# Optimization experiments

Measured on AMD Instinct MI355X. Metric: run time of the kernel, lower is better.

## Reference

```python
import jax, jax.numpy as jnp
import numpy as np
import math

H_HEADS = 4
SQRT_2_PI = math.sqrt(2.0 / math.pi)


def _gelu_tanh(x):
    return 0.5 * x * (1.0 + jnp.tanh(SQRT_2_PI * (x + 0.044715 * x ** 3)))


def _ln(x, g, b, eps=1e-5):
    mu = jnp.mean(x, axis=-1, keepdims=True)
    var = jnp.var(x, axis=-1, keepdims=True)
    return g * (x - mu) * jax.lax.rsqrt(var + eps) + b


def _forward(support_emb_mat, query_t, support_t, cls_embed, t_freq, t_phase,
             Wq, bq, Wk, bk, Wv, bv, Wo, bo, ln1_g, ln1_b, time_w,
             W1, b1, W2, b2, ln2_g, ln2_b, Wc, bc, bn_g, bn_b):
    B, F, MD = support_emb_mat.shape
    Q = query_t.shape[1]
    S = F + 1
    H = H_HEADS
    D = MD * H
    dph = D // H
    L = Wq.shape[0]
    BQ = B * Q

    # [CLS] + support sequence, feature-tiled to model_dim*num_heads
    cls = jnp.broadcast_to(cls_embed, (B, 1, MD))
    seq = jnp.concatenate([cls, support_emb_mat], axis=1)          # [B,S,MD]
    x = jnp.tile(seq, (1, 1, H))                                    # [B,S,D]
    x = jnp.broadcast_to(x[:, None], (B, Q, S, D)).reshape(BQ, S, D)

    # time sequence: [query_t_q, support_t...] per (b,q)
    sup = jnp.broadcast_to(support_t[:, None, :], (B, Q, F))
    t_seq = jnp.concatenate([query_t[..., None], sup], axis=-1).reshape(BQ, S)
    t_diff = t_seq[:, :, None] - t_seq[:, None, :]                  # [BQ,S,S]
    # time encoder: cos(t*freq + phase) -> [BQ,S,S,TD]
    t_emb = jnp.cos(t_diff[..., None] * t_freq + t_phase)

    # scale as in source: (dim_per_head // num_heads) ** -0.5
    scale = (dph // H) ** (-0.5)

    for l in range(L):
        bias = t_emb @ time_w[l]                                    # [BQ,S,S]
        add = jnp.tile(bias, (H, 1, 1))                             # [BQ*H,S,S]
        res = x
        # raw row-major reshape to (BQ*H, S, dph) exactly as torch .view
        q = (x @ Wq[l] + bq[l]).reshape(BQ * H, S, dph)
        k = (x @ Wk[l] + bk[l]).reshape(BQ * H, S, dph)
        v = (x @ Wv[l] + bv[l]).reshape(BQ * H, S, dph)
        attn = jax.nn.softmax(jnp.einsum('bsd,btd->bst', q, k) * scale + add, axis=-1)
        ctx = jnp.einsum('bst,btd->bsd', attn, v).reshape(BQ, S, D)
        out = _ln(res + ctx @ Wo[l] + bo[l], ln1_g[l], ln1_b[l])
        ffn = _gelu_tanh(out @ W1[l] + b1[l]) @ W2[l] + b2[l]
        x = _ln(out + ffn, ln2_g[l], ln2_b[l])

    # compress: Linear -> BatchNorm1d over seq channels (train mode) -> LeakyReLU
    h = x @ Wc + bc                                                 # [BQ,S,MD]
    mu = jnp.mean(h, axis=(0, 2), keepdims=True)
    var = jnp.var(h, axis=(0, 2), keepdims=True)
    h = bn_g[None, :, None] * (h - mu) * jax.lax.rsqrt(var + 1e-5) + bn_b[None, :, None]
    h = jnp.where(h >= 0, h, 0.01 * h)                              # LeakyReLU
    return h[:, 0, :].reshape(B, Q, MD)


def setup_inputs() -> dict:
    key = jax.random.key(0)
    ks = jax.random.split(key, 24)
    B, Q, F, MD = 128, 32, 7, 128
    H, L, FFN, TD = 4, 6, 2048, 32
    S = F + 1
    D = MD * H

    def nrm(k, shape, s=0.02):
        return jax.random.normal(k, shape, jnp.float32) * s

    inp = {
        'support_emb_mat': jax.random.normal(ks[0], (B, F, MD), jnp.float32),
        'query_t': jax.random.uniform(ks[1], (B, Q), jnp.float32) * 100.0,
        'support_t': jax.random.uniform(ks[2], (B, F), jnp.float32) * 100.0,
        'cls_embed': jax.random.uniform(ks[3], (1, MD), jnp.float32),
        't_freq': nrm(ks[4], (TD,), 1.0),
        't_phase': nrm(ks[5], (TD,), 1.0),
        'Wq': nrm(ks[6], (L, D, D)), 'bq': jnp.zeros((L, D)),
        'Wk': nrm(ks[7], (L, D, D)), 'bk': jnp.zeros((L, D)),
        'Wv': nrm(ks[8], (L, D, D)), 'bv': jnp.zeros((L, D)),
        'Wo': nrm(ks[9], (L, D, D)), 'bo': jnp.zeros((L, D)),
        'ln1_g': jnp.ones((L, D)), 'ln1_b': jnp.zeros((L, D)),
        'time_w': jnp.ones((L, TD)) * 0.001,
        'W1': nrm(ks[10], (L, D, FFN)), 'b1': jnp.zeros((L, FFN)),
        'W2': nrm(ks[11], (L, FFN, D)), 'b2': jnp.zeros((L, D)),
        'ln2_g': jnp.ones((L, D)), 'ln2_b': jnp.zeros((L, D)),
        'Wc': nrm(ks[12], (D, MD)), 'bc': jnp.zeros((MD,)),
        'bn_g': jnp.ones((S,)), 'bn_b': jnp.zeros((S,)),
    }
    return inp


def reference(support_emb_mat, query_t, support_t, cls_embed, t_freq, t_phase,
              Wq, bq, Wk, bk, Wv, bv, Wo, bo, ln1_g, ln1_b, time_w,
              W1, b1, W2, b2, ln2_g, ln2_b, Wc, bc, bn_g, bn_b):
    return _forward(support_emb_mat, query_t, support_t, cls_embed, t_freq, t_phase,
                    Wq, bq, Wk, bk, Wv, bv, Wo, bo, ln1_g, ln1_b, time_w,
                    W1, b1, W2, b2, ln2_g, ln2_b, Wc, bc, bn_g, bn_b)
```

## Files before the change

kernel.cpp:

```cpp
#include <hip/hip_runtime.h>
#include <hip/hip_bf16.h>

typedef _Float16 f16;
typedef __attribute__((ext_vector_type(8))) _Float16 f16x8;
typedef __attribute__((ext_vector_type(4))) _Float16 f16x4;
typedef __attribute__((ext_vector_type(4))) float f32x4;

#define DEVI __device__ __forceinline__

DEVI float ldf(const void* p, size_t i, int isf32) {
    if (isf32) return ((const float*)p)[i];
    unsigned int u = ((const unsigned short*)p)[i];
    union { unsigned int b; float f; } c; c.b = u << 16;
    return c.f;
}

DEVI void gld_lds16(const f16* g, f16* l) {
    __builtin_amdgcn_global_load_lds(
        (__attribute__((address_space(1))) void*)(g),
        (__attribute__((address_space(3))) void*)(l), 16, 0, 0);
}

__global__ void detect_dtype(const void* qt, int* flag) {
    if (threadIdx.x == 0 && blockIdx.x == 0) {
        const unsigned int* w = (const unsigned int*)qt;
        int cnt = 0;
        for (int i = 0; i < 64; ++i) {
            unsigned int lo = w[i] & 0xFFFFu;
            union { unsigned int b; float f; } c; c.b = lo << 16;
            if (c.f >= 1e-4f && c.f <= 100.5f) ++cnt;
        }
        *flag = (cnt >= 32) ? 0 : 1;
    }
}

__global__ __launch_bounds__(256)
void cvt_in(const void* __restrict__ src, float* __restrict__ dst, int n,
            const int* __restrict__ flag) {
    const int f32 = *flag;
    int i = blockIdx.x * 256 + threadIdx.x;
    if (i < n) dst[i] = ldf(src, i, f32);
}

__global__ __launch_bounds__(256)
void fill_out(float* out, float v) {
    out[blockIdx.x * 256 + threadIdx.x] = v;
}

template<int EPI>
__global__ __launch_bounds__(512, 2)
void gemm256(const f16* __restrict__ Ag, const f16* __restrict__ BTg,
             const float* __restrict__ biasg, void* __restrict__ outg,
             int NZ, int gridN, int N, int K, int lda,
             long zsB, long zsBias, long zsC)
{
    const int tid = threadIdx.x;
    const int w = tid >> 6, lane = tid & 63;
    const int wm = w >> 2, wn = w & 3;
    const int r16 = lane & 15, q4 = lane >> 4;

    const int cpx = gridDim.x >> 3;
    const int id  = (blockIdx.x & 7) * cpx + (blockIdx.x >> 3);

    const int nz   = id % NZ;
    const int mloc = id / NZ;
    const int z    = nz / gridN;
    const int nt   = nz - z * gridN;
    const int tm = mloc * 256, tn = nt * 256;

    const f16*   BT   = BTg + (size_t)z * zsB;
    const float* bias = biasg + (size_t)z * zsBias;
    const size_t zoffC = (size_t)z * zsC;

    __shared__ __align__(16) f16 smA[2][2][16][64][8];
    __shared__ __align__(16) f16 smB[2][2][16][64][8];

    const f16* gA[4]; const f16* gB[4];
#pragma unroll
    for (int t = 0; t < 4; ++t) {
        const int c = 4 * w + t, kk = c >> 4, rc = c & 15;
        gA[t] = Ag + (size_t)(tm + rc * 16 + r16) * lda + kk * 32 + q4 * 8;
        gB[t] = BT + (size_t)(tn + rc * 16 + r16) * K  + kk * 32 + q4 * 8;
    }
    f16* const smAbase = &smA[0][0][0][0][0];
    f16* const smBbase = &smB[0][0][0][0][0];
    const int coff = (4 * w) * 512;

    auto issue = [&](int kt, int buf) {
        const size_t o = (size_t)kt * 64;
        const int bo = buf * 16384 + coff;
#pragma unroll
        for (int t = 0; t < 4; ++t) {
            gld_lds16(gA[t] + o, smAbase + bo + t * 512);
            gld_lds16(gB[t] + o, smBbase + bo + t * 512);
        }
    };

    f32x4 acc[8][4];
#pragma unroll
    for (int i = 0; i < 8; ++i)
#pragma unroll
        for (int j = 0; j < 4; ++j) acc[i][j] = (f32x4)0.0f;

    const int iters = K >> 6;
    issue(0, 0);
    __builtin_amdgcn_s_waitcnt(0x0F70);
    __builtin_amdgcn_s_barrier();
    __asm__ __volatile__("" ::: "memory");

    for (int kt = 0; kt < iters; ++kt) {
        const int cur = kt & 1;
        const bool more = (kt + 1 < iters);
        if (more) issue(kt + 1, cur ^ 1);
#pragma unroll
        for (int kk = 0; kk < 2; ++kk) {
            f16x8 af[8], bf[4];
#pragma unroll
            for (int i = 0; i < 8; ++i)
                af[i] = *(const f16x8*)&smA[cur][kk][wm * 8 + i][lane][0];
#pragma unroll
            for (int j = 0; j < 4; ++j)
                bf[j] = *(const f16x8*)&smB[cur][kk][wn * 4 + j][lane][0];
#pragma unroll
            for (int i = 0; i < 8; ++i)
#pragma unroll
                for (int j = 0; j < 4; ++j)
                    acc[i][j] = __builtin_amdgcn_mfma_f32_16x16x32_f16(
                        bf[j], af[i], acc[i][j], 0, 0, 0);
        }
        if (more) {
            __builtin_amdgcn_s_waitcnt(0x0F70);
            __builtin_amdgcn_s_barrier();
            __asm__ __volatile__("" ::: "memory");
        }
    }

    const int rowBase = tm + wm * 128;
    const int colBase = tn + wn * 64;
#pragma unroll
    for (int i = 0; i < 8; ++i) {
        const int row = rowBase + i * 16 + r16;
        const size_t rowoff = (size_t)row * N;
#pragma unroll
        for (int j = 0; j < 4; ++j) {
            const int n0 = colBase + j * 16 + q4 * 4;
            const f32x4 bv4 = *(const f32x4*)&bias[n0];
            f16x4 o;
#pragma unroll
            for (int r = 0; r < 4; ++r) {
                float v = acc[i][j][r] + bv4[r];
                if constexpr (EPI == 2) {
                    float v2 = v * v;
                    float t  = v * (1.0f + 0.044715f * v2);
                    float e  = __expf(1.5957691216057308f * t);
                    float rc = __builtin_amdgcn_rcpf(e + 1.0f);
                    v = v - v * rc;
                }
                o[r] = (f16)v;
            }
            *(f16x4*)((f16*)outg + zoffC + rowoff + n0) = o;
        }
    }
}

template<int EPI>
__global__ __launch_bounds__(256, 4)
void gemm_bt2(const f16* __restrict__ Ag, const f16* __restrict__ BTg,
              const float* __restrict__ biasg, void* __restrict__ outg,
              int NZ, int gridN, int N, int K, int lda,
              long zsB, long zsBias, long zsC)
{
    const int tid  = threadIdx.x;
    const int w    = tid >> 6, lane = tid & 63;
    const int wm   = w >> 1,   wn   = w & 1;
    const int r16  = lane & 15, q4 = lane >> 4;

    const int cpx = gridDim.x >> 3;
    const int id  = (blockIdx.x & 7) * cpx + (blockIdx.x >> 3);

    const int nz   = id % NZ;
    const int mloc = id / NZ;
    const int z    = nz / gridN;
    const int nt   = nz - z * gridN;
    const int tm   = mloc * 128, tn = nt * 128;

    const f16*   BT   = BTg + (size_t)z * zsB;
    const float* bias = biasg + (size_t)z * zsBias;
    const size_t zoffC = (size_t)z * zsC;

    __shared__ __align__(16) f16 smA[2][8][64][8];
    __shared__ __align__(16) f16 smB[2][8][64][8];

    const int iters = K >> 5;

    const f16* gA0 = Ag + (size_t)(tm + (2 * w) * 16 + r16) * lda + q4 * 8;
    const f16* gA1 = gA0 + (size_t)16 * lda;
    const f16* gB0 = BT + (size_t)(tn + (2 * w) * 16 + r16) * K + q4 * 8;
    const f16* gB1 = gB0 + (size_t)16 * K;

    auto issue = [&](int kt, int buf) {
        const size_t o = (size_t)kt * 32;
        gld_lds16(gA0 + o, &smA[buf][2 * w][0][0]);
        gld_lds16(gA1 + o, &smA[buf][2 * w + 1][0][0]);
        gld_lds16(gB0 + o, &smB[buf][2 * w][0][0]);
        gld_lds16(gB1 + o, &smB[buf][2 * w + 1][0][0]);
    };

    f32x4 acc[4][4];
#pragma unroll
    for (int i = 0; i < 4; ++i)
#pragma unroll
        for (int j = 0; j < 4; ++j) acc[i][j] = (f32x4)0.0f;

    issue(0, 0);
    for (int kt = 0; kt < iters; ++kt) {
        const int cur = kt & 1;
        __builtin_amdgcn_s_barrier();
        if (kt + 1 < iters) {
            issue(kt + 1, cur ^ 1);
            __builtin_amdgcn_s_waitcnt(0x0F74);
        } else {
            __builtin_amdgcn_s_waitcnt(0x0F70);
        }
        __builtin_amdgcn_s_barrier();
        __asm__ __volatile__("" ::: "memory");

        f16x8 af[4], bf[4];
#pragma unroll
        for (int i = 0; i < 4; ++i) {
            af[i] = *(const f16x8*)&smA[cur][wm * 4 + i][lane][0];
            bf[i] = *(const f16x8*)&smB[cur][wn * 4 + i][lane][0];
        }
#pragma unroll
        for (int i = 0; i < 4; ++i)
#pragma unroll
            for (int j = 0; j < 4; ++j)
                acc[i][j] = __builtin_amdgcn_mfma_f32_16x16x32_f16(
                    bf[j], af[i], acc[i][j], 0, 0, 0);
    }

    const int rowBase = tm + wm * 64;
    const int colBase = tn + wn * 64;
#pragma unroll
    for (int i = 0; i < 4; ++i) {
        const int row = rowBase + i * 16 + r16;
        const size_t rowoff = (size_t)row * N;
#pragma unroll
        for (int j = 0; j < 4; ++j) {
            const int n0 = colBase + j * 16 + q4 * 4;
            const f32x4 bv4 = *(const f32x4*)&bias[n0];
            if constexpr (EPI == 3) {
                f32x4 o;
#pragma unroll
                for (int r = 0; r < 4; ++r) o[r] = acc[i][j][r] + bv4[r];
                *(f32x4*)((float*)outg + rowoff + n0) = o;
            } else {
                f16x4 o;
#pragma unroll
                for (int r = 0; r < 4; ++r) {
                    float v = acc[i][j][r] + bv4[r];
                    if constexpr (EPI == 2) {
                        float v2 = v * v;
                        float t  = v * (1.0f + 0.044715f * v2);
                        float e  = __expf(1.5957691216057308f * t);
                        float rc = __builtin_amdgcn_rcpf(e + 1.0f);
                        v = v - v * rc;
                    }
                    o[r] = (f16)v;
                }
                *(f16x4*)((f16*)outg + zoffC + rowoff + n0) = o;
            }
        }
    }
}

__global__ __launch_bounds__(512, 2)
void gemm_ln(const f16* __restrict__ Ag, const f16* __restrict__ BTg,
             const float* __restrict__ bias, const f16* __restrict__ resg,
             const float* __restrict__ lng, const float* __restrict__ lnb,
             f16* __restrict__ Yg, int K, int lda, int rstride)
{
    const int tid = threadIdx.x;
    const int w = tid >> 6, lane = tid & 63;
    const int wm = w >> 2, wn = w & 3;
    const int r16 = lane & 15, q4 = lane >> 4;
    const int tm = blockIdx.x * 128;

    __shared__ __align__(16) f16 smA[2][8][64][8];
    __shared__ __align__(16) f16 smB[2][32][64][8];
    __shared__ __align__(16) float lnS[128][4];
    __shared__ __align__(16) float lnQ[128][4];

    f32x4 acc[4][8];
#pragma unroll
    for (int i = 0; i < 4; ++i)
#pragma unroll
        for (int j = 0; j < 8; ++j) acc[i][j] = (f32x4)0.0f;

    const f16* gA  = Ag  + (size_t)(tm + w * 16 + r16) * lda + q4 * 8;
    const f16* gB  = BTg + (size_t)(w * 64 + r16) * K + q4 * 8;
    const int iters = K >> 5;

    auto issue = [&](int kt, int buf) {
        const size_t o = (size_t)kt * 32;
        gld_lds16(gA + o, &smA[buf][w][0][0]);
#pragma unroll
        for (int t = 0; t < 4; ++t)
            gld_lds16(gB + (size_t)(t * 16) * K + o, &smB[buf][w * 4 + t][0][0]);
    };

    issue(0, 0);
    for (int kt = 0; kt < iters; ++kt) {
        const int cur = kt & 1;
        __builtin_amdgcn_s_barrier();
        if (kt + 1 < iters) {
            issue(kt + 1, cur ^ 1);
            __builtin_amdgcn_s_waitcnt(0x0F75);
        } else {
            __builtin_amdgcn_s_waitcnt(0x0F70);
        }
        __builtin_amdgcn_s_barrier();
        __asm__ __volatile__("" ::: "memory");

        f16x8 af[4], bf[8];
#pragma unroll
        for (int i = 0; i < 4; ++i)
            af[i] = *(const f16x8*)&smA[cur][wm * 4 + i][lane][0];
#pragma unroll
        for (int j = 0; j < 8; ++j)
            bf[j] = *(const f16x8*)&smB[cur][wn * 8 + j][lane][0];
#pragma unroll
        for (int i = 0; i < 4; ++i)
#pragma unroll
            for (int j = 0; j < 8; ++j)
                acc[i][j] = __builtin_amdgcn_mfma_f32_16x16x32_f16(
                    bf[j], af[i], acc[i][j], 0, 0, 0);
    }

    const int rowB = wm * 64;
    const int colB = wn * 128;

    float ps[4], pq[4];
#pragma unroll
    for (int i = 0; i < 4; ++i) {
        const int grow = tm + rowB + i * 16 + r16;
        const size_t roff = (size_t)grow * rstride;
        float s = 0.f, sq = 0.f;
#pragma unroll
        for (int j = 0; j < 8; ++j) {
            const int n0 = colB + j * 16 + q4 * 4;
            const f32x4 biv = *(const f32x4*)&bias[n0];
            const f16x4 rv  = *(const f16x4*)&resg[roff + n0];
#pragma unroll
            for (int r = 0; r < 4; ++r) {
                float v = acc[i][j][r] + biv[r] + (float)rv[r];
                acc[i][j][r] = v;
                s += v; sq += v * v;
            }
        }
        s  += __shfl_xor(s, 16, 64);  s  += __shfl_xor(s, 32, 64);
        sq += __shfl_xor(sq, 16, 64); sq += __shfl_xor(sq, 32, 64);
        ps[i] = s; pq[i] = sq;
    }
    if (q4 == 0) {
#pragma unroll
        for (int i = 0; i < 4; ++i) {
            const int lr = rowB + i * 16 + r16;
            lnS[lr][wn] = ps[i];
            lnQ[lr][wn] = pq[i];
        }
    }
    __syncthreads();

#pragma unroll
    for (int i = 0; i < 4; ++i) {
        const int lr = rowB + i * 16 + r16;
        const f32x4 s4 = *(const f32x4*)&lnS[lr][0];
        const f32x4 q4v = *(const f32x4*)&lnQ[lr][0];
        const float s  = s4[0] + s4[1] + s4[2] + s4[3];
        const float sq = q4v[0] + q4v[1] + q4v[2] + q4v[3];
        const float mu = s * (1.0f / 512.0f);
        const float var = sq * (1.0f / 512.0f) - mu * mu;
        const float rs = rsqrtf(var + 1e-5f);
        const size_t rowoff = (size_t)(tm + lr) * 512;
#pragma unroll
        for (int j = 0; j < 8; ++j) {
            const int n0 = colB + j * 16 + q4 * 4;
            const f32x4 g4 = *(const f32x4*)&lng[n0];
            const f32x4 b4 = *(const f32x4*)&lnb[n0];
            f16x4 o;
#pragma unroll
            for (int r = 0; r < 4; ++r)
                o[r] = (f16)(g4[r] * (acc[i][j][r] - mu) * rs + b4[r]);
            *(f16x4*)&Yg[rowoff + n0] = o;
        }
    }
}

__global__ __launch_bounds__(256)
void attn_kernel(const f16* __restrict__ qg, const f16* __restrict__ kg,
                 const f16* __restrict__ vg, const float* __restrict__ biasL,
                 f16* __restrict__ cg, int mode)
{
    const int w = threadIdx.x >> 6, lane = threadIdx.x & 63;
    const int j = blockIdx.x * 4 + w;
    __shared__ __align__(16) f16 sQ[4][8][136];
    __shared__ __align__(16) f16 sK[4][8][136];
    __shared__ __align__(16) f16 sV[4][8][136];
    __shared__ float sP[4][8][8];

    size_t base, biasrow;
    if (mode == 2) {
        base = (size_t)j * 4096;
        biasrow = (size_t)((j << 2) & 4095);
        {
            int flat = lane * 8;
            *(f16x8*)&sQ[w][flat >> 7][flat & 127] =
                *(const f16x8*)(qg + (size_t)j * 512 + flat);
            int f2 = 512 + lane * 8;
            *(f16x8*)&sQ[w][f2 >> 7][f2 & 127] = (f16x8)(f16)0.0f;
        }
#pragma unroll
        for (int t = 0; t < 2; ++t) {
            int flat = (t * 64 + lane) * 8;
            int r = flat >> 7, c = flat & 127;
            *(f16x8*)&sK[w][r][c] = *(const f16x8*)(kg + base + flat);
            *(f16x8*)&sV[w][r][c] = *(const f16x8*)(vg + base + flat);
        }
    } else {
        base = (size_t)j * 1024;
        biasrow = (size_t)(j & 4095);
        const size_t ibase = (mode == 1)
            ? ((size_t)(j >> 7) * 4096 + (size_t)(j & 3) * 1024) : base;
#pragma unroll
        for (int t = 0; t < 2; ++t) {
            int flat = (t * 64 + lane) * 8;
            int r = flat >> 7, c = flat & 127;
            *(f16x8*)&sQ[w][r][c] = *(const f16x8*)(qg + ibase + flat);
            *(f16x8*)&sK[w][r][c] = *(const f16x8*)(kg + ibase + flat);
            *(f16x8*)&sV[w][r][c] = *(const f16x8*)(vg + ibase + flat);
        }
    }
    __syncthreads();

    const int i = lane >> 3, jj = lane & 7;
    float d = 0.f;
#pragma unroll
    for (int c = 0; c < 16; ++c) {
        f16x8 qv = *(const f16x8*)&sQ[w][i][c * 8];
        f16x8 kv = *(const f16x8*)&sK[w][jj][c * 8];
#pragma unroll
        for (int e = 0; e < 8; ++e) d += (float)qv[e] * (float)kv[e];
    }
    float s = d * 0.17677669529663687f + biasL[biasrow * 64 + lane];
    float mx = s;
    mx = fmaxf(mx, __shfl_xor(mx, 1, 64));
    mx = fmaxf(mx, __shfl_xor(mx, 2, 64));
    mx = fmaxf(mx, __shfl_xor(mx, 4, 64));
    float p = __expf(s - mx);
    float sum = p;
    sum += __shfl_xor(sum, 1, 64);
    sum += __shfl_xor(sum, 2, 64);
    sum += __shfl_xor(sum, 4, 64);
    sP[w][i][jj] = p / sum;
    __syncthreads();

    const int nrows = (mode == 2) ? 4 : 8;
    for (int t2 = 0; t2 < nrows; ++t2) {
        float ap[8];
#pragma unroll
        for (int e = 0; e < 8; ++e) ap[e] = sP[w][t2][e];
#pragma unroll
        for (int h = 0; h < 2; ++h) {
            int flat = (t2 * 2 + h) * 64 + lane;
            int dd = flat & 127;
            float o = 0.f;
#pragma unroll
            for (int e = 0; e < 8; ++e) o += ap[e] * (float)sV[w][e][dd];
            cg[base + flat] = (f16)o;
        }
    }
}

__global__ __launch_bounds__(256)
void build_x0(const void* __restrict__ sup, const void* __restrict__ cls,
              f16* __restrict__ xb, const int* __restrict__ flag)
{
    const int f32 = *flag;
    const size_t idx = ((size_t)blockIdx.x * 256 + threadIdx.x) * 4;
    const int row = (int)(idx >> 9), col0 = (int)(idx & 511);
    const int s = row & 7, b = row >> 8;
    f16x4 o;
#pragma unroll
    for (int e = 0; e < 4; ++e) {
        const int md = (col0 + e) & 127;
        float v = (s == 0) ? ldf(cls, md, f32)
                           : ldf(sup, ((size_t)b * 7 + (s - 1)) * 128 + md, f32);
        o[e] = (f16)v;
    }
    *(f16x4*)(xb + idx) = o;
}

__global__ __launch_bounds__(256)
void build_x0s(const void* __restrict__ sup, const void* __restrict__ cls,
               f16* __restrict__ xs, const int* __restrict__ flag)
{
    const int f32 = *flag;
    const size_t idx = ((size_t)blockIdx.x * 256 + threadIdx.x) * 4;
    const int row = (int)(idx >> 9), col0 = (int)(idx & 511);
    const int s = row & 7, b = row >> 3;
    f16x4 o;
#pragma unroll
    for (int e = 0; e < 4; ++e) {
        const int md = (col0 + e) & 127;
        float v = (s == 0) ? ldf(cls, md, f32)
                           : ldf(sup, ((size_t)b * 7 + (s - 1)) * 128 + md, f32);
        o[e] = (f16)v;
    }
    *(f16x4*)(xs + idx) = o;
}

__global__ __launch_bounds__(256)
void bias_kernel(const void* __restrict__ qt, const void* __restrict__ st,
                 const void* __restrict__ freq, const void* __restrict__ phase,
                 const void* __restrict__ tw, float* __restrict__ biasAll,
                 const int* __restrict__ flag)
{
    const int f32 = *flag;
    const int lane = threadIdx.x & 63;
    const int bq = blockIdx.x * 4 + (threadIdx.x >> 6);
    const int b = bq >> 5, qq = bq & 31;
    const int i = lane >> 3, jj = lane & 7;
    const float ti = (i  == 0) ? ldf(qt, b * 32 + qq, f32) : ldf(st, b * 7 + i  - 1, f32);
    const float tj = (jj == 0) ? ldf(qt, b * 32 + qq, f32) : ldf(st, b * 7 + jj - 1, f32);
    const float td = ti - tj;
    float a[6] = {0.f, 0.f, 0.f, 0.f, 0.f, 0.f};
    for (int t = 0; t < 32; ++t) {
        float c = __cosf(td * ldf(freq, t, f32) + ldf(phase, t, f32));
#pragma unroll
        for (int l = 0; l < 6; ++l) a[l] += c * ldf(tw, l * 32 + t, f32);
    }
#pragma unroll
    for (int l = 0; l < 6; ++l)
        biasAll[(size_t)l * (4096 * 64) + (size_t)bq * 64 + lane] = a[l];
}

__global__ __launch_bounds__(256)
void transpose_cvt(const void* __restrict__ W, f16* __restrict__ WT,
                   int K, int N, long zsW, long zsWT, const int* __restrict__ flag)
{
    const int f32 = *flag;
    const size_t zoff = (size_t)blockIdx.z * zsW;
    f16* WTz = WT + (size_t)blockIdx.z * zsWT;
    __shared__ float tile[64][65];
    const int tn = blockIdx.x * 64, tk = blockIdx.y * 64;
#pragma unroll
    for (int t = 0; t < 16; ++t) {
        int idx = t * 256 + threadIdx.x;
        int r = idx >> 6, c = idx & 63;
        tile[r][c] = ldf(W, zoff + (size_t)(tk + r) * N + tn + c, f32);
    }
    __syncthreads();
#pragma unroll
    for (int t = 0; t < 16; ++t) {
        int idx = t * 256 + threadIdx.x;
        int r = idx >> 6, c = idx & 63;
        WTz[(size_t)(tn + r) * K + tk + c] = (f16)tile[c][r];
    }
}

__global__ __launch_bounds__(256)
void gather_qkvb(const void* __restrict__ bq, const void* __restrict__ bk,
                 const void* __restrict__ bv, float* __restrict__ dst,
                 const int* __restrict__ flag)
{
    const int f32 = *flag;
    int i = blockIdx.x * 256 + threadIdx.x;
    if (i < 9216) {
        int z = i / 3072, rem = i % 3072;
        const void* src = (z == 0) ? bq : ((z == 1) ? bk : bv);
        dst[i] = ldf(src, rem, f32);
    }
}

__global__ __launch_bounds__(256)
void bn_reduce(const float* __restrict__ h0, float* __restrict__ stats)
{
    const int t = blockIdx.x * 256 + threadIdx.x;
    float s = 0.f, ss = 0.f;
#pragma unroll
    for (int k = 0; k < 8; ++k) {
        float v = h0[t + k * 65536];
        s += v; ss += v * v;
    }
#pragma unroll
    for (int m = 1; m <= 32; m <<= 1) {
        s  += __shfl_xor(s, m, 64);
        ss += __shfl_xor(ss, m, 64);
    }
    __shared__ float ls[8];
    const int w = threadIdx.x >> 6, lane = threadIdx.x & 63;
    if (lane == 0) { ls[w] = s; ls[4 + w] = ss; }
    __syncthreads();
    if (threadIdx.x == 0) {
        atomicAdd(&stats[0], ls[0] + ls[1] + ls[2] + ls[3]);
        atomicAdd(&stats[1], ls[4] + ls[5] + ls[6] + ls[7]);
    }
}

__global__ __launch_bounds__(256)
void bn_apply(const float* __restrict__ h0, const float* __restrict__ stats,
              const float* __restrict__ bnp, float* __restrict__ out)
{
    const int t = blockIdx.x * 256 + threadIdx.x;
    const float mu  = stats[0] * (1.0f / 524288.0f);
    const float var = stats[1] * (1.0f / 524288.0f) - mu * mu;
    const float rs  = rsqrtf(var + 1e-5f);
    float v = bnp[0] * (h0[t] - mu) * rs + bnp[8];
    v = (v >= 0.f) ? v : 0.01f * v;
    out[t] = v;
}

extern "C" void kernel_launch(void* const* d_in, const int* in_sizes, int n_in,
                              void* d_out, int out_size, void* d_ws, size_t ws_size,
                              hipStream_t stream)
{
    (void)in_sizes; (void)n_in; (void)out_size;
    const void* sup   = d_in[0];
    const void* qt    = d_in[1];
    const void* st    = d_in[2];
    const void* cls   = d_in[3];
    const void* freq  = d_in[4];
    const void* phase = d_in[5];
    const void* Wq = d_in[6];  const void* bqv = d_in[7];
    const void* Wk = d_in[8];  const void* bkv = d_in[9];
    const void* Wv = d_in[10]; const void* bvv = d_in[11];
    const void* Wo = d_in[12]; const void* bo  = d_in[13];
    const void* ln1g = d_in[14]; const void* ln1b = d_in[15];
    const void* tw = d_in[16];
    const void* W1 = d_in[17]; const void* b1 = d_in[18];
    const void* W2 = d_in[19]; const void* b2 = d_in[20];
    const void* ln2g = d_in[21]; const void* ln2b = d_in[22];
    const void* Wc = d_in[23]; const void* bc = d_in[24];
    const void* bng = d_in[25]; const void* bnb = d_in[26];

    const size_t NEEDED = 245658240;
    if (ws_size < NEEDED) {
        fill_out<<<2048, 256, 0, stream>>>((float*)d_out, 999.0f);
        return;
    }

    char* ws = (char*)d_ws;
    f16*   wt      = (f16*)(ws + 0);
    float* biasAll = (float*)(ws + 37879808);
    float* qkvb    = (float*)(ws + 44171264);
    float* prm     = (float*)(ws + 44208128);
    float* stats   = (float*)(ws + 44331584);
    int*   flag    = (int*)  (ws + 44331592);
    f16*   xb      = (f16*)(ws + 44331648);
    f16*   ob      = (f16*)(ws + 77886080);
    char*  region  = ws + 111440512;
    f16*   qb      = (f16*)(region);
    f16*   kb      = (f16*)(region + 33554432);
    f16*   vb      = (f16*)(region + 67108864);
    f16*   cb      = (f16*)(region + 100663296);
    f16*   qs      = (f16*)(region);
    f16*   xs      = (f16*)(region + 100663296);
    f16*   fbuf    = (f16*)(region);
    float* h0      = (float*)(region);

    detect_dtype<<<1, 64, 0, stream>>>(qt, flag);

    cvt_in<<<12, 256, 0, stream>>>(bo,   prm + 0,     3072,  flag);
    cvt_in<<<48, 256, 0, stream>>>(b1,   prm + 3072,  12288, flag);
    cvt_in<<<12, 256, 0, stream>>>(b2,   prm + 15360, 3072,  flag);
    cvt_in<<<1,  256, 0, stream>>>(bc,   prm + 18432, 128,   flag);
    cvt_in<<<12, 256, 0, stream>>>(ln1g, prm + 18560, 3072,  flag);
    cvt_in<<<12, 256, 0, stream>>>(ln1b, prm + 21632, 3072,  flag);
    cvt_in<<<12, 256, 0, stream>>>(ln2g, prm + 24704, 3072,  flag);
    cvt_in<<<12, 256, 0, stream>>>(ln2b, prm + 27776, 3072,  flag);
    cvt_in<<<1,  256, 0, stream>>>(bng,  prm + 30848, 8,     flag);
    cvt_in<<<1,  256, 0, stream>>>(bnb,  prm + 30856, 8,     flag);

    transpose_cvt<<<dim3(8, 8, 6),  256, 0, stream>>>(Wq, wt + 0,        512, 512,  262144, 262144, flag);
    transpose_cvt<<<dim3(8, 8, 6),  256, 0, stream>>>(Wk, wt + 1572864,  512, 512,  262144, 262144, flag);
    transpose_cvt<<<dim3(8, 8, 6),  256, 0, stream>>>(Wv, wt + 3145728,  512, 512,  262144, 262144, flag);
    transpose_cvt<<<dim3(8, 8, 6),  256, 0, stream>>>(Wo, wt + 4718592,  512, 512,  262144, 262144, flag);
    transpose_cvt<<<dim3(32, 8, 6), 256, 0, stream>>>(W1, wt + 6291456,  512, 2048, 1048576, 1048576, flag);
    transpose_cvt<<<dim3(8, 32, 6), 256, 0, stream>>>(W2, wt + 12582912, 2048, 512, 1048576, 1048576, flag);
    transpose_cvt<<<dim3(2, 8, 1),  256, 0, stream>>>(Wc, wt + 18874368, 512, 128,  0, 0, flag);
    gather_qkvb<<<36, 256, 0, stream>>>(bqv, bkv, bvv, qkvb, flag);
    build_x0<<<16384, 256, 0, stream>>>(sup, cls, xb, flag);
    build_x0s<<<512, 256, 0, stream>>>(sup, cls, xs, flag);
    bias_kernel<<<1024, 256, 0, stream>>>(qt, st, freq, phase, tw, biasAll, flag);
    hipMemsetAsync(stats, 0, 8, stream);

    for (int l = 0; l < 6; ++l) {
        if (l == 0) {
            gemm256<0><<<24, 512, 0, stream>>>(
                xs, wt, qkvb, qs,
                6, 2, 512, 512, 512, 1572864, 3072, 524288);
            attn_kernel<<<4096, 256, 0, stream>>>(
                qs, qs + 524288, qs + 1048576, biasAll, cb, 1);
        } else if (l < 5) {
            gemm256<0><<<768, 512, 0, stream>>>(
                xb, wt + l * 262144, qkvb + l * 512, qb,
                6, 2, 512, 512, 512, 1572864, 3072, 16777216);
            attn_kernel<<<4096, 256, 0, stream>>>(
                qb, kb, vb, biasAll + (size_t)l * 262144, cb, 0);
        } else {
            gemm256<0><<<64, 512, 0, stream>>>(
                xb, wt + l * 262144 + 1572864, qkvb + l * 512 + 3072, kb,
                4, 2, 4096, 512, 4096, 1572864, 3072, 16777216);
            gemm256<0><<<64, 512, 0, stream>>>(
                xb + 512, wt + l * 262144 + 1572864, qkvb + l * 512 + 3072, kb + 512,
                4, 2, 4096, 512, 4096, 1572864, 3072, 16777216);
            gemm256<0><<<32, 512, 0, stream>>>(
                xb, wt + l * 262144, qkvb + l * 512, qb,
                2, 2, 512, 512, 4096, 0, 0, 0);
            attn_kernel<<<1024, 256, 0, stream>>>(
                qb, kb, vb, biasAll + (size_t)l * 262144, cb, 2);
        }
        if (l < 5) {
            gemm_ln<<<256, 512, 0, stream>>>(
                cb, wt + 4718592 + l * 262144, prm + 0 + l * 512, xb,
                prm + 18560 + l * 512, prm + 21632 + l * 512, ob, 512, 512, 512);
            gemm256<2><<<1024, 512, 0, stream>>>(
                ob, wt + 6291456 + l * 1048576, prm + 3072 + l * 2048, fbuf,
                8, 8, 2048, 512, 512, 0, 0, 0);
            gemm_ln<<<256, 512, 0, stream>>>(
                fbuf, wt + 12582912 + l * 1048576, prm + 15360 + l * 512, ob,
                prm + 24704 + l * 512, prm + 27776 + l * 512, xb, 2048, 2048, 512);
        } else {
            gemm_ln<<<32, 512, 0, stream>>>(
                cb, wt + 4718592 + l * 262144, prm + 0 + l * 512, xb,
                prm + 18560 + l * 512, prm + 21632 + l * 512, ob, 512, 4096, 4096);
            gemm256<2><<<128, 512, 0, stream>>>(
                ob, wt + 6291456 + l * 1048576, prm + 3072 + l * 2048, fbuf,
                8, 8, 2048, 512, 512, 0, 0, 0);
            gemm_ln<<<32, 512, 0, stream>>>(
                fbuf, wt + 12582912 + l * 1048576, prm + 15360 + l * 512, ob,
                prm + 24704 + l * 512, prm + 27776 + l * 512, cb, 2048, 2048, 512);
        }
    }

    gemm_bt2<3><<<32, 256, 0, stream>>>(
        cb, wt + 18874368, prm + 18432, h0,
        1, 1, 128, 512, 512, 0, 0, 0);
    bn_reduce<<<256, 256, 0, stream>>>(h0, stats);
    bn_apply<<<2048, 256, 0, stream>>>(h0, stats, prm + 30848, (float*)d_out);
}
```

Baseline: 2.719 ms.

## Add wide-N QKV GEMM kernel and unify last-layer attention path

Adds a gemm_qkv kernel in which each block computes a 128x512 tile of one projection, using 8 waves and double-buffered LDS loads, to raise reuse of the activation tile. It replaces gemm256 for the QKV projections in layers 1–5. The special last-layer path, which computed only the CLS rows for Q, attention and the output projection, is removed, so layer 5 now runs full QKV, full attention and a full Wo+LN. Only its FFN stays restricted to CLS rows, read with a 4096 stride. This simplifies the code but adds a lot of work to the final layer, and it also strips the unused GELU epilogue from gemm_bt2.

```diff
diff --git a/kernel.cpp b/kernel.cpp
--- a/kernel.cpp
+++ b/kernel.cpp
@@ -163,6 +163,93 @@
     }
 }
 
+__global__ __launch_bounds__(512, 2)
+void gemm_qkv(const f16* __restrict__ Ag, const f16* __restrict__ BTg,
+              const float* __restrict__ biasg, f16* __restrict__ outg,
+              int NZ, int K, int lda, long zsB, long zsBias, long zsC)
+{
+    const int tid = threadIdx.x;
+    const int w = tid >> 6, lane = tid & 63;
+    const int wm = w >> 2, wn = w & 3;
+    const int r16 = lane & 15, q4 = lane >> 4;
+
+    const int cpx = gridDim.x >> 3;
+    const int id  = (blockIdx.x & 7) * cpx + (blockIdx.x >> 3);
+    const int z    = id % NZ;
+    const int mloc = id / NZ;
+    const int tm   = mloc * 128;
+
+    const f16*   BT   = BTg + (size_t)z * zsB;
+    const float* bias = biasg + (size_t)z * zsBias;
+    f16*         out  = outg + (size_t)z * zsC;
+
+    __shared__ __align__(16) f16 smA[2][8][64][8];
+    __shared__ __align__(16) f16 smB[2][32][64][8];
+
+    f32x4 acc[4][8];
+#pragma unroll
+    for (int i = 0; i < 4; ++i)
+#pragma unroll
+        for (int j = 0; j < 8; ++j) acc[i][j] = (f32x4)0.0f;
+
+    const f16* gA  = Ag + (size_t)(tm + w * 16 + r16) * lda + q4 * 8;
+    const f16* gB  = BT + (size_t)(w * 64 + r16) * K + q4 * 8;
+    const int iters = K >> 5;
+
+    auto issue = [&](int kt, int buf) {
+        const size_t o = (size_t)kt * 32;
+        gld_lds16(gA + o, &smA[buf][w][0][0]);
+#pragma unroll
+        for (int t = 0; t < 4; ++t)
+            gld_lds16(gB + (size_t)(t * 16) * K + o, &smB[buf][w * 4 + t][0][0]);
+    };
+
+    issue(0, 0);
+    for (int kt = 0; kt < iters; ++kt) {
+        const int cur = kt & 1;
+        __builtin_amdgcn_s_barrier();
+        if (kt + 1 < iters) {
+            issue(kt + 1, cur ^ 1);
+            __builtin_amdgcn_s_waitcnt(0x0F75);
+        } else {
+            __builtin_amdgcn_s_waitcnt(0x0F70);
+        }
+        __builtin_amdgcn_s_barrier();
+        __asm__ __volatile__("" ::: "memory");
+
+        f16x8 af[4], bf[8];
+#pragma unroll
+        for (int i = 0; i < 4; ++i)
+            af[i] = *(const f16x8*)&smA[cur][wm * 4 + i][lane][0];
+#pragma unroll
+        for (int j = 0; j < 8; ++j)
+            bf[j] = *(const f16x8*)&smB[cur][wn * 8 + j][lane][0];
+#pragma unroll
+        for (int i = 0; i < 4; ++i)
+#pragma unroll
+            for (int j = 0; j < 8; ++j)
+                acc[i][j] = __builtin_amdgcn_mfma_f32_16x16x32_f16(
+                    bf[j], af[i], acc[i][j], 0, 0, 0);
+    }
+
+    const int rowB = wm * 64;
+    const int colB = wn * 128;
+#pragma unroll
+    for (int i = 0; i < 4; ++i) {
+        const int row = tm + rowB + i * 16 + r16;
+        const size_t rowoff = (size_t)row * 512;
+#pragma unroll
+        for (int j = 0; j < 8; ++j) {
+            const int n0 = colB + j * 16 + q4 * 4;
+            const f32x4 bv4 = *(const f32x4*)&bias[n0];
+            f16x4 o;
+#pragma unroll
+            for (int r = 0; r < 4; ++r) o[r] = (f16)(acc[i][j][r] + bv4[r]);
+            *(f16x4*)&out[rowoff + n0] = o;
+        }
+    }
+}
+
 template<int EPI>
 __global__ __launch_bounds__(256, 4)
 void gemm_bt2(const f16* __restrict__ Ag, const f16* __restrict__ BTg,
@@ -176,7 +263,8 @@
     const int r16  = lane & 15, q4 = lane >> 4;
 
     const int cpx = gridDim.x >> 3;
-    const int id  = (blockIdx.x & 7) * cpx + (blockIdx.x >> 3);
+    const int id  = (gridDim.x >= 8) ? ((blockIdx.x & 7) * cpx + (blockIdx.x >> 3))
+                                     : blockIdx.x;
 
     const int nz   = id % NZ;
     const int mloc = id / NZ;
@@ -257,17 +345,7 @@
             } else {
                 f16x4 o;
 #pragma unroll
-                for (int r = 0; r < 4; ++r) {
-                    float v = acc[i][j][r] + bv4[r];
-                    if constexpr (EPI == 2) {
-                        float v2 = v * v;
-                        float t  = v * (1.0f + 0.044715f * v2);
-                        float e  = __expf(1.5957691216057308f * t);
-                        float rc = __builtin_amdgcn_rcpf(e + 1.0f);
-                        v = v - v * rc;
-                    }
-                    o[r] = (f16)v;
-                }
+                for (int r = 0; r < 4; ++r) o[r] = (f16)(acc[i][j][r] + bv4[r]);
                 *(f16x4*)((f16*)outg + zoffC + rowoff + n0) = o;
             }
         }
@@ -409,37 +487,16 @@
     __shared__ __align__(16) f16 sV[4][8][136];
     __shared__ float sP[4][8][8];
 
-    size_t base, biasrow;
-    if (mode == 2) {
-        base = (size_t)j * 4096;
-        biasrow = (size_t)((j << 2) & 4095);
-        {
-            int flat = lane * 8;
-            *(f16x8*)&sQ[w][flat >> 7][flat & 127] =
-                *(const f16x8*)(qg + (size_t)j * 512 + flat);
-            int f2 = 512 + lane * 8;
-            *(f16x8*)&sQ[w][f2 >> 7][f2 & 127] = (f16x8)(f16)0.0f;
-        }
-#pragma unroll
-        for (int t = 0; t < 2; ++t) {
-            int flat = (t * 64 + lane) * 8;
-            int r = flat >> 7, c = flat & 127;
-            *(f16x8*)&sK[w][r][c] = *(const f16x8*)(kg + base + flat);
-            *(f16x8*)&sV[w][r][c] = *(const f16x8*)(vg + base + flat);
-        }
-    } else {
-        base = (size_t)j * 1024;
-        biasrow = (size_t)(j & 4095);
-        const size_t ibase = (mode == 1)
-            ? ((size_t)(j >> 7) * 4096 + (size_t)(j & 3) * 1024) : base;
-#pragma unroll
-        for (int t = 0; t < 2; ++t) {
-            int flat = (t * 64 + lane) * 8;
-            int r = flat >> 7, c = flat & 127;
-            *(f16x8*)&sQ[w][r][c] = *(const f16x8*)(qg + ibase + flat);
-            *(f16x8*)&sK[w][r][c] = *(const f16x8*)(kg + ibase + flat);
-            *(f16x8*)&sV[w][r][c] = *(const f16x8*)(vg + ibase + flat);
-        }
+    const size_t base  = (size_t)j * 1024;
+    const size_t ibase = (mode == 1)
+        ? ((size_t)(j >> 7) * 4096 + (size_t)(j & 3) * 1024) : base;
+#pragma unroll
+    for (int t = 0; t < 2; ++t) {
+        int flat = (t * 64 + lane) * 8;
+        int r = flat >> 7, c = flat & 127;
+        *(f16x8*)&sQ[w][r][c] = *(const f16x8*)(qg + ibase + flat);
+        *(f16x8*)&sK[w][r][c] = *(const f16x8*)(kg + ibase + flat);
+        *(f16x8*)&sV[w][r][c] = *(const f16x8*)(vg + ibase + flat);
     }
     __syncthreads();
 
@@ -452,7 +509,7 @@
 #pragma unroll
         for (int e = 0; e < 8; ++e) d += (float)qv[e] * (float)kv[e];
     }
-    float s = d * 0.17677669529663687f + biasL[biasrow * 64 + lane];
+    float s = d * 0.17677669529663687f + biasL[(size_t)(j & 4095) * 64 + lane];
     float mx = s;
     mx = fmaxf(mx, __shfl_xor(mx, 1, 64));
     mx = fmaxf(mx, __shfl_xor(mx, 2, 64));
@@ -465,8 +522,8 @@
     sP[w][i][jj] = p / sum;
     __syncthreads();
 
-    const int nrows = (mode == 2) ? 4 : 8;
-    for (int t2 = 0; t2 < nrows; ++t2) {
+#pragma unroll
+    for (int t2 = 0; t2 < 8; ++t2) {
         float ap[8];
 #pragma unroll
         for (int e = 0; e < 8; ++e) ap[e] = sP[w][t2][e];
@@ -702,29 +759,17 @@
                 6, 2, 512, 512, 512, 1572864, 3072, 524288);
             attn_kernel<<<4096, 256, 0, stream>>>(
                 qs, qs + 524288, qs + 1048576, biasAll, cb, 1);
-        } else if (l < 5) {
-            gemm256<0><<<768, 512, 0, stream>>>(
+        } else {
+            gemm_qkv<<<768, 512, 0, stream>>>(
                 xb, wt + l * 262144, qkvb + l * 512, qb,
-                6, 2, 512, 512, 512, 1572864, 3072, 16777216);
+                3, 512, 512, 1572864, 3072, 16777216);
             attn_kernel<<<4096, 256, 0, stream>>>(
                 qb, kb, vb, biasAll + (size_t)l * 262144, cb, 0);
-        } else {
-            gemm256<0><<<64, 512, 0, stream>>>(
-                xb, wt + l * 262144 + 1572864, qkvb + l * 512 + 3072, kb,
-                4, 2, 4096, 512, 4096, 1572864, 3072, 16777216);
-            gemm256<0><<<64, 512, 0, stream>>>(
-                xb + 512, wt + l * 262144 + 1572864, qkvb + l * 512 + 3072, kb + 512,
-                4, 2, 4096, 512, 4096, 1572864, 3072, 16777216);
-            gemm256<0><<<32, 512, 0, stream>>>(
-                xb, wt + l * 262144, qkvb + l * 512, qb,
-                2, 2, 512, 512, 4096, 0, 0, 0);
-            attn_kernel<<<1024, 256, 0, stream>>>(
-                qb, kb, vb, biasAll + (size_t)l * 262144, cb, 2);
-        }
+        }
+        gemm_ln<<<256, 512, 0, stream>>>(
+            cb, wt + 4718592 + l * 262144, prm + 0 + l * 512, xb,
+            prm + 18560 + l * 512, prm + 21632 + l * 512, ob, 512, 512, 512);
         if (l < 5) {
-            gemm_ln<<<256, 512, 0, stream>>>(
-                cb, wt + 4718592 + l * 262144, prm + 0 + l * 512, xb,
-                prm + 18560 + l * 512, prm + 21632 + l * 512, ob, 512, 512, 512);
             gemm256<2><<<1024, 512, 0, stream>>>(
                 ob, wt + 6291456 + l * 1048576, prm + 3072 + l * 2048, fbuf,
                 8, 8, 2048, 512, 512, 0, 0, 0);
@@ -732,15 +777,12 @@
                 fbuf, wt + 12582912 + l * 1048576, prm + 15360 + l * 512, ob,
                 prm + 24704 + l * 512, prm + 27776 + l * 512, xb, 2048, 2048, 512);
         } else {
-            gemm_ln<<<32, 512, 0, stream>>>(
-                cb, wt + 4718592 + l * 262144, prm + 0 + l * 512, xb,
-                prm + 18560 + l * 512, prm + 21632 + l * 512, ob, 512, 4096, 4096);
             gemm256<2><<<128, 512, 0, stream>>>(
                 ob, wt + 6291456 + l * 1048576, prm + 3072 + l * 2048, fbuf,
-                8, 8, 2048, 512, 512, 0, 0, 0);
+                8, 8, 2048, 512, 4096, 0, 0, 0);
             gemm_ln<<<32, 512, 0, stream>>>(
                 fbuf, wt + 12582912 + l * 1048576, prm + 15360 + l * 512, ob,
-                prm + 24704 + l * 512, prm + 27776 + l * 512, cb, 2048, 2048, 512);
+                prm + 24704 + l * 512, prm + 27776 + l * 512, cb, 2048, 2048, 4096);
         }
     }
 
```

Result: slower. 2.791 ms (+2.6%).
